# Kernel optimization log

Measured on AMD Instinct MI355X. Metric: run time of the kernel, lower is better.

Reference implementation:

```python
import jax, jax.numpy as jnp
import numpy as np

N = 100000      # nodes
E = 1600000     # edges
G = 1000        # graphs in the batch
D_IN, D_H, D_OUT = 128, 128, 64


def setup_inputs() -> dict:
    key = jax.random.key(0)
    ks = jax.random.split(key, 8)
    x = jax.random.normal(ks[0], (N, D_IN), jnp.float32)
    edge_index = jax.random.randint(ks[1], (2, E), 0, N, dtype=jnp.int32)
    batch = jnp.sort(jax.random.randint(ks[2], (N,), 0, G, dtype=jnp.int32))
    s_in = 1.0 / np.sqrt(D_IN)
    s_h = 1.0 / np.sqrt(D_H)
    return {
        "x": x,
        "edge_index": edge_index,
        "batch": batch,
        "W_emb": jax.random.normal(ks[3], (D_IN, D_H), jnp.float32) * s_in,
        "b_emb": jnp.zeros((D_H,), jnp.float32),
        "W1": jax.random.normal(ks[4], (D_H, D_H), jnp.float32) * s_h,
        "b1": jnp.zeros((D_H,), jnp.float32),
        "W2": jax.random.normal(ks[5], (D_H, D_H), jnp.float32) * s_h,
        "b2": jnp.zeros((D_H,), jnp.float32),
        "W3": jax.random.normal(ks[6], (D_H, D_OUT), jnp.float32) * s_h,
        "b3": jnp.zeros((D_OUT,), jnp.float32),
    }


def reference(x, edge_index, batch, W_emb, b_emb, W1, b1, W2, b2, W3, b3):
    # Eval mode: dropout is identity.
    n = x.shape[0]
    src, dst = edge_index[0], edge_index[1]
    # GCN symmetric normalization with self-loops (Kipf & Welling).
    deg = jax.ops.segment_sum(jnp.ones(src.shape[0], x.dtype), dst, num_segments=n) + 1.0
    dis = jax.lax.rsqrt(deg)                 # deg^{-1/2}, [N]
    edge_norm = dis[src] * dis[dst]          # [E]
    self_norm = dis * dis                    # self-loop weight = 1/deg, [N]

    def gcn_conv(h, W, b):
        h = h @ W                                         # [N, d_out]
        agg = jax.ops.segment_sum(h[src] * edge_norm[:, None], dst, num_segments=n)
        return agg + h * self_norm[:, None] + b

    h = x @ W_emb + b_emb
    h = jax.nn.relu(gcn_conv(h, W1, b1))
    h = jax.nn.relu(gcn_conv(h, W2, b2))
    h = gcn_conv(h, W3, b3)
    # global_add_pool over graph ids
    return jax.ops.segment_sum(h, batch, num_segments=G)
```

## Files before the change

kernel.cpp:

```cpp
#include <hip/hip_runtime.h>
#include <hip/hip_bf16.h>

#define NN 100000
#define NE 1600000
#define NG 1000
#define SMAX 48

typedef unsigned short u16;
typedef unsigned int u32;
typedef u16 u16x8 __attribute__((ext_vector_type(8)));
typedef u32 u32x4 __attribute__((ext_vector_type(4)));
typedef float f32x4 __attribute__((ext_vector_type(4)));
typedef __attribute__((ext_vector_type(8))) short s16x8;
typedef __attribute__((ext_vector_type(4))) float facc4;

__device__ __forceinline__ float bf2f(u16 u) {
    union { u32 i; float f; } c; c.i = ((u32)u) << 16; return c.f;
}
__device__ __forceinline__ u16 f2bf(float f) {
    __hip_bfloat16 h = __float2bfloat16(f);
    union { __hip_bfloat16 h; u16 u; } c; c.h = h; return c.u;
}
__device__ __forceinline__ int ntload(const int* p) { return __builtin_nontemporal_load(p); }

__global__ __launch_bounds__(256) void detect_kernel(const u32* __restrict__ xr, int* __restrict__ flag) {
    __shared__ int cnt[256];
    int c = 0;
    for (int i = threadIdx.x; i < 4096; i += 256) {
        u32 e = (xr[i] >> 7) & 0xFFu;
        if (e >= 110u && e <= 135u) c++;
    }
    cnt[threadIdx.x] = c;
    __syncthreads();
    for (int o = 128; o > 0; o >>= 1) {
        if (threadIdx.x < o) cnt[threadIdx.x] += cnt[threadIdx.x + o];
        __syncthreads();
    }
    if (threadIdx.x == 0) flag[0] = (cnt[0] > 2048) ? 1 : 0;
}

#define MEGA_NB 12726
__global__ __launch_bounds__(256) void mega_prep(
    const void* __restrict__ x, const int* __restrict__ flag, u16* __restrict__ xb,
    const void* __restrict__ Wemb, const void* __restrict__ W1, const void* __restrict__ W2,
    const void* __restrict__ W3, u16* __restrict__ wembT, u16* __restrict__ w1T,
    u16* __restrict__ w2T, u16* __restrict__ w3T,
    const void* __restrict__ bemb, const void* __restrict__ b1, const void* __restrict__ b2,
    const void* __restrict__ b3, float* __restrict__ bembF, float* __restrict__ b1F,
    float* __restrict__ b2F, float* __restrict__ b3F,
    const int* __restrict__ ei, int* __restrict__ counts)
{
    int b = blockIdx.x, tid = threadIdx.x;
    int fl = flag[0];
    if (b < 6250) {
        if (fl) return;
        int c = b * 256 + tid;
        f32x4 a = reinterpret_cast<const f32x4*>(x)[c * 2];
        f32x4 d = reinterpret_cast<const f32x4*>(x)[c * 2 + 1];
        u16x8 o;
        #pragma unroll
        for (int j = 0; j < 4; ++j) { o[j] = f2bf(a[j]); o[4 + j] = f2bf(d[j]); }
        reinterpret_cast<u16x8*>(xb)[c] = o;
    } else if (b < 6474) {
        int o = (b - 6250) * 256 + tid;
        const void* src; u16* dst; int M; int ol;
        if (o < 16384)      { src = Wemb; dst = wembT; M = 128; ol = o; }
        else if (o < 32768) { src = W1;   dst = w1T;   M = 128; ol = o - 16384; }
        else if (o < 49152) { src = W2;   dst = w2T;   M = 128; ol = o - 32768; }
        else                { src = W3;   dst = w3T;   M = 64;  ol = o - 49152; }
        int n = ol >> 7, k = ol & 127;
        u16 v = fl ? reinterpret_cast<const u16*>(src)[k * M + n]
                   : f2bf(reinterpret_cast<const float*>(src)[k * M + n]);
        dst[ol] = v;
    } else if (b < 6476) {
        int i = (b - 6474) * 256 + tid;
        if (i >= 448) return;
        const void* src; float* dst; int il;
        if (i < 128)      { src = bemb; dst = bembF; il = i; }
        else if (i < 256) { src = b1;   dst = b1F;   il = i - 128; }
        else if (i < 384) { src = b2;   dst = b2F;   il = i - 256; }
        else              { src = b3;   dst = b3F;   il = i - 384; }
        dst[il] = fl ? bf2f(reinterpret_cast<const u16*>(src)[il])
                     : reinterpret_cast<const float*>(src)[il];
    } else {
        int e = (b - 6476) * 256 + tid;
        if (e < NE) atomicAdd(&counts[ei[NE + e]], 1);
    }
}

__global__ __launch_bounds__(256) void wfuse_kernel(const u16* __restrict__ w1T, const u16* __restrict__ wembT,
                                                    const float* __restrict__ bembF,
                                                    u16* __restrict__ WfT, float* __restrict__ bfW) {
    int b = blockIdx.x;
    if (b < 64) {
        int o = b * 256 + threadIdx.x;
        int n = o >> 7, k = o & 127;
        float acc = 0.f;
        #pragma unroll 4
        for (int j = 0; j < 128; ++j)
            acc += bf2f(w1T[n * 128 + j]) * bf2f(wembT[j * 128 + k]);
        WfT[o] = f2bf(acc);
    } else {
        int n = threadIdx.x;
        if (n < 128) {
            float acc = 0.f;
            for (int j = 0; j < 128; ++j)
                acc += bembF[j] * bf2f(w1T[n * 128 + j]);
            bfW[n] = acc;
        }
    }
}

__global__ __launch_bounds__(256) void scan1_kernel(const int* __restrict__ counts, int* __restrict__ offs,
                                                    int* __restrict__ bsums, float* __restrict__ dis,
                                                    int* __restrict__ cursor) {
    __shared__ int sums[256];
    int tid = threadIdx.x;
    int base = blockIdx.x * 2048 + tid * 8;
    int local[8];
    int s = 0;
    #pragma unroll
    for (int i = 0; i < 8; ++i) {
        int v = 0;
        if (base + i < NN) {
            v = counts[base + i];
            dis[base + i] = rsqrtf((float)v + 1.0f);
            cursor[base + i] = 0;
        }
        local[i] = s; s += v;
    }
    sums[tid] = s;
    __syncthreads();
    for (int o = 1; o < 256; o <<= 1) {
        int v = (tid >= o) ? sums[tid - o] : 0;
        __syncthreads();
        sums[tid] += v;
        __syncthreads();
    }
    int excl = sums[tid] - s;
    #pragma unroll
    for (int i = 0; i < 8; ++i)
        if (base + i < NN) offs[base + i] = excl + local[i];
    if (tid == 255) bsums[blockIdx.x] = sums[255];
}

__global__ __launch_bounds__(256) void scan3_kernel(int* __restrict__ offs, const int* __restrict__ bsums) {
    __shared__ int addv;
    int i = blockIdx.x * 256 + threadIdx.x;
    int bucket = blockIdx.x >> 3;
    if (threadIdx.x == 0) {
        int s = 0;
        for (int k = 0; k < bucket; ++k) s += bsums[k];
        addv = s;
    }
    __syncthreads();
    if (i < NN) offs[i] += addv;
}

#define MEGA2_SCAT 6250
__global__ __launch_bounds__(256, 5) void mega2_kernel(
    const u16* __restrict__ xb, const u16* __restrict__ xraw, const int* __restrict__ flag,
    const u16* __restrict__ WfT, const float* __restrict__ bfW, u16* __restrict__ Hout,
    const int* __restrict__ ei, const int* __restrict__ offs, int* __restrict__ cursor,
    int* __restrict__ srcs)
{
    int b = blockIdx.x, tid = threadIdx.x;
    if (b < MEGA2_SCAT) {
        int e = b * 256 + tid;
        if (e < NE) {
            int s = ei[e], d = ei[NE + e];
            int pos = offs[d] + atomicAdd(&cursor[d], 1);
            srcs[pos] = s;
        }
    } else {
        const u16* A = flag[0] ? xraw : xb;
        int gb = b - MEGA2_SCAT;
        int wv = tid >> 6, lane = tid & 63;
        int m = lane & 15, quad = lane >> 4;
        int r0 = gb * 64 + wv * 16;
        int ar = r0 + m; if (ar >= NN) ar = NN - 1;
        facc4 acc[8];
        #pragma unroll
        for (int t = 0; t < 8; ++t) acc[t] = (facc4){0.f, 0.f, 0.f, 0.f};
        const u16* arow = A + (size_t)ar * 128 + quad * 8;
        #pragma unroll
        for (int k0 = 0; k0 < 128; k0 += 32) {
            s16x8 a = *reinterpret_cast<const s16x8*>(arow + k0);
            #pragma unroll
            for (int t = 0; t < 8; ++t) {
                s16x8 bfr = *reinterpret_cast<const s16x8*>(WfT + (t * 16 + m) * 128 + k0 + quad * 8);
                acc[t] = __builtin_amdgcn_mfma_f32_16x16x32_bf16(a, bfr, acc[t], 0, 0, 0);
            }
        }
        #pragma unroll
        for (int t = 0; t < 8; ++t) {
            int col = t * 16 + m;
            float bv = bfW[col];
            #pragma unroll
            for (int r = 0; r < 4; ++r) {
                int orow = r0 + quad * 4 + r;
                if (orow < NN)
                    Hout[(size_t)orow * 128 + col] = f2bf(acc[t][r] + bv);
            }
        }
    }
}

template <int MOUT>
__global__ __launch_bounds__(256) void fused_agg_gemm(const u16* __restrict__ T, const int* __restrict__ offs,
                                                      const int* __restrict__ counts, const float* __restrict__ dis,
                                                      const int* __restrict__ srcs, const float* __restrict__ aggbias,
                                                      const u16* __restrict__ Wt, u16* __restrict__ Hout) {
    constexpr int LDW = 136;
    __shared__ u16 sW[MOUT * LDW];
    __shared__ u16 sA[64 * LDW];
    int tid = threadIdx.x;
    for (int c = tid; c < MOUT * 16; c += 256) {
        int n = c >> 4, kc = (c & 15) << 3;
        *reinterpret_cast<u16x8*>(sW + n * LDW + kc) = reinterpret_cast<const u16x8*>(Wt)[c];
    }

    int lane = tid & 15, grp = tid >> 4;
    const u32x4* T4 = reinterpret_cast<const u32x4*>(T);
    for (int i = 0; i < 4; ++i) {
        int nl = grp * 4 + i;
        int n = blockIdx.x * 64 + nl;
        bool valid = n < NN;
        int nc = valid ? n : NN - 1;
        float di = dis[nc];
        float sn = di * di;
        u32x4 ts = T4[(size_t)nc * 16 + lane];
        float acc[8];
        #pragma unroll
        for (int q = 0; q < 4; ++q) {
            acc[2 * q]     = bf2f((u16)(ts[q] & 0xffffu)) * sn + aggbias[lane * 8 + 2 * q];
            acc[2 * q + 1] = bf2f((u16)(ts[q] >> 16))     * sn + aggbias[lane * 8 + 2 * q + 1];
        }
        int st = offs[nc], cnt = valid ? counts[nc] : 0;
        int j = 0;
        for (; j + 4 <= cnt; j += 4) {
            int e0 = ntload(srcs + st + j);
            int e1 = ntload(srcs + st + j + 1);
            int e2 = ntload(srcs + st + j + 2);
            int e3 = ntload(srcs + st + j + 3);
            float w0 = dis[e0] * di, w1 = dis[e1] * di, w2 = dis[e2] * di, w3 = dis[e3] * di;
            u32x4 g0 = T4[(size_t)e0 * 16 + lane];
            u32x4 g1 = T4[(size_t)e1 * 16 + lane];
            u32x4 g2 = T4[(size_t)e2 * 16 + lane];
            u32x4 g3 = T4[(size_t)e3 * 16 + lane];
            #pragma unroll
            for (int q = 0; q < 4; ++q) {
                acc[2 * q]     += bf2f((u16)(g0[q] & 0xffffu)) * w0;
                acc[2 * q + 1] += bf2f((u16)(g0[q] >> 16))     * w0;
                acc[2 * q]     += bf2f((u16)(g1[q] & 0xffffu)) * w1;
                acc[2 * q + 1] += bf2f((u16)(g1[q] >> 16))     * w1;
                acc[2 * q]     += bf2f((u16)(g2[q] & 0xffffu)) * w2;
                acc[2 * q + 1] += bf2f((u16)(g2[q] >> 16))     * w2;
                acc[2 * q]     += bf2f((u16)(g3[q] & 0xffffu)) * w3;
                acc[2 * q + 1] += bf2f((u16)(g3[q] >> 16))     * w3;
            }
        }
        for (; j < cnt; ++j) {
            int e = ntload(srcs + st + j);
            float w = dis[e] * di;
            u32x4 g = T4[(size_t)e * 16 + lane];
            #pragma unroll
            for (int q = 0; q < 4; ++q) {
                acc[2 * q]     += bf2f((u16)(g[q] & 0xffffu)) * w;
                acc[2 * q + 1] += bf2f((u16)(g[q] >> 16))     * w;
            }
        }
        u16x8 pk;
        #pragma unroll
        for (int q = 0; q < 4; ++q) {
            pk[2 * q]     = f2bf(fmaxf(acc[2 * q], 0.0f));
            pk[2 * q + 1] = f2bf(fmaxf(acc[2 * q + 1], 0.0f));
        }
        *reinterpret_cast<u16x8*>(sA + nl * LDW + lane * 8) = pk;
    }
    __syncthreads();

    int wv = tid >> 6, l64 = tid & 63;
    int m = l64 & 15, quad = l64 >> 4;
    int r0 = blockIdx.x * 64 + wv * 16;
    constexpr int NT = MOUT / 16;
    facc4 gacc[NT];
    #pragma unroll
    for (int t = 0; t < NT; ++t) gacc[t] = (facc4){0.f, 0.f, 0.f, 0.f};
    #pragma unroll
    for (int k0 = 0; k0 < 128; k0 += 32) {
        s16x8 a = *reinterpret_cast<const s16x8*>(sA + (wv * 16 + m) * LDW + k0 + quad * 8);
        #pragma unroll
        for (int t = 0; t < NT; ++t) {
            s16x8 bfr = *reinterpret_cast<const s16x8*>(sW + (t * 16 + m) * LDW + k0 + quad * 8);
            gacc[t] = __builtin_amdgcn_mfma_f32_16x16x32_bf16(a, bfr, gacc[t], 0, 0, 0);
        }
    }
    #pragma unroll
    for (int t = 0; t < NT; ++t) {
        int col = t * 16 + m;
        #pragma unroll
        for (int r = 0; r < 4; ++r) {
            int orow = r0 + quad * 4 + r;
            if (orow < NN)
                Hout[(size_t)orow * MOUT + col] = f2bf(gacc[t][r]);
        }
    }
}

__global__ __launch_bounds__(256) void agg_pool_kernel(const u16* __restrict__ T, const int* __restrict__ offs,
                                                       const int* __restrict__ counts, const float* __restrict__ dis,
                                                       const int* __restrict__ srcs, const float* __restrict__ bias,
                                                       const int* __restrict__ batch, float* __restrict__ outF) {
    __shared__ float accG[SMAX * 64];
    __shared__ int sg0;
    int tid = threadIdx.x;
    for (int i = tid; i < SMAX * 64; i += 256) accG[i] = 0.0f;
    if (tid == 0) sg0 = batch[blockIdx.x * 32];
    __syncthreads();
    int g0 = sg0;
    int lane = tid & 7;
    int n = blockIdx.x * 32 + (tid >> 3);

    const u32x4* T4 = reinterpret_cast<const u32x4*>(T);
    float di = dis[n];
    float sn = di * di;
    u32x4 ts = T4[(size_t)n * 8 + lane];
    float acc[8];
    #pragma unroll
    for (int q = 0; q < 4; ++q) {
        acc[2 * q]     = bf2f((u16)(ts[q] & 0xffffu)) * sn + bias[lane * 8 + 2 * q];
        acc[2 * q + 1] = bf2f((u16)(ts[q] >> 16))     * sn + bias[lane * 8 + 2 * q + 1];
    }
    int st = offs[n], cnt = counts[n];
    int j = 0;
    for (; j + 4 <= cnt; j += 4) {
        int e0 = ntload(srcs + st + j);
        int e1 = ntload(srcs + st + j + 1);
        int e2 = ntload(srcs + st + j + 2);
        int e3 = ntload(srcs + st + j + 3);
        float w0 = dis[e0] * di, w1 = dis[e1] * di, w2 = dis[e2] * di, w3 = dis[e3] * di;
        u32x4 g0v = T4[(size_t)e0 * 8 + lane];
        u32x4 g1v = T4[(size_t)e1 * 8 + lane];
        u32x4 g2v = T4[(size_t)e2 * 8 + lane];
        u32x4 g3v = T4[(size_t)e3 * 8 + lane];
        #pragma unroll
        for (int q = 0; q < 4; ++q) {
            acc[2 * q]     += bf2f((u16)(g0v[q] & 0xffffu)) * w0;
            acc[2 * q + 1] += bf2f((u16)(g0v[q] >> 16))     * w0;
            acc[2 * q]     += bf2f((u16)(g1v[q] & 0xffffu)) * w1;
            acc[2 * q + 1] += bf2f((u16)(g1v[q] >> 16))     * w1;
            acc[2 * q]     += bf2f((u16)(g2v[q] & 0xffffu)) * w2;
            acc[2 * q + 1] += bf2f((u16)(g2v[q] >> 16))     * w2;
            acc[2 * q]     += bf2f((u16)(g3v[q] & 0xffffu)) * w3;
            acc[2 * q + 1] += bf2f((u16)(g3v[q] >> 16))     * w3;
        }
    }
    for (; j < cnt; ++j) {
        int e = ntload(srcs + st + j);
        float w = dis[e] * di;
        u32x4 g = T4[(size_t)e * 8 + lane];
        #pragma unroll
        for (int q = 0; q < 4; ++q) {
            acc[2 * q]     += bf2f((u16)(g[q] & 0xffffu)) * w;
            acc[2 * q + 1] += bf2f((u16)(g[q] >> 16))     * w;
        }
    }

    int s = batch[n] - g0;
    if (s >= 0 && s < SMAX) {
        #pragma unroll
        for (int q = 0; q < 8; ++q)
            atomicAdd(&accG[s * 64 + lane * 8 + q], acc[q]);
    } else {
        #pragma unroll
        for (int q = 0; q < 8; ++q)
            atomicAdd(&outF[(size_t)(g0 + s) * 64 + lane * 8 + q], acc[q]);
    }
    __syncthreads();
    int gend = batch[blockIdx.x * 32 + 31];
    int span = gend - g0 + 1;
    if (span > SMAX) span = SMAX;
    for (int i = tid; i < span * 64; i += 256)
        atomicAdd(&outF[(size_t)g0 * 64 + i], accG[i]);
}

__global__ __launch_bounds__(256) void out_cvt_kernel(const float* __restrict__ outF, void* __restrict__ out,
                                                      const int* __restrict__ flag) {
    int i = blockIdx.x * 256 + threadIdx.x;
    if (i < NG * 64) {
        float v = outF[i];
        if (flag[0]) reinterpret_cast<u16*>(out)[i] = f2bf(v);
        else         reinterpret_cast<float*>(out)[i] = v;
    }
}

extern "C" void kernel_launch(void* const* d_in, const int* in_sizes, int n_in,
                              void* d_out, int out_size, void* d_ws, size_t ws_size,
                              hipStream_t stream) {
    const void* x     = d_in[0];
    const int* ei     = (const int*)d_in[1];
    const int* batch  = (const int*)d_in[2];
    const void* W_emb = d_in[3];
    const void* b_emb = d_in[4];
    const void* W1    = d_in[5];
    const void* b1    = d_in[6];
    const void* W2    = d_in[7];
    const void* b2    = d_in[8];
    const void* W3    = d_in[9];
    const void* b3    = d_in[10];

    char* p = (char*)d_ws;
    auto alloc = [&](size_t bytes) { void* r = p; p += (bytes + 255) & ~(size_t)255; return r; };
    int*   flag   = (int*)alloc(256);
    int*   counts = (int*)alloc(NN * 4);
    int*   cursor = (int*)alloc(NN * 4);
    int*   offs   = (int*)alloc(NN * 4);
    float* dis    = (float*)alloc(NN * 4);
    int*   bsums  = (int*)alloc(256 * 4);
    int*   srcs   = (int*)alloc((size_t)NE * 4);
    u16*   wembT  = (u16*)alloc(128 * 128 * 2);
    u16*   w1T    = (u16*)alloc(128 * 128 * 2);
    u16*   w2T    = (u16*)alloc(128 * 128 * 2);
    u16*   w3T    = (u16*)alloc(64 * 128 * 2);
    u16*   WfT    = (u16*)alloc(128 * 128 * 2);
    float* bembF  = (float*)alloc(128 * 4);
    float* b1F    = (float*)alloc(128 * 4);
    float* b2F    = (float*)alloc(128 * 4);
    float* b3F    = (float*)alloc(64 * 4);
    float* bfW    = (float*)alloc(128 * 4);
    float* outF   = (float*)alloc((size_t)NG * 64 * 4);
    u16*   hA     = (u16*)alloc((size_t)(NN + 64) * 128 * 2);
    u16*   hB     = (u16*)alloc((size_t)(NN + 64) * 128 * 2);

    hipMemsetAsync(counts, 0, NN * 4, stream);
    hipMemsetAsync(outF, 0, (size_t)NG * 64 * 4, stream);

    const int SB = (NN + 2047) / 2048;
    const int NB = (NN + 255) / 256;
    const int GB = (NN + 63) / 64;

    detect_kernel<<<1, 256, 0, stream>>>((const u32*)x, flag);
    mega_prep<<<MEGA_NB, 256, 0, stream>>>(x, flag, hB, W_emb, W1, W2, W3, wembT, w1T, w2T, w3T,
                                           b_emb, b1, b2, b3, bembF, b1F, b2F, b3F, ei, counts);
    wfuse_kernel<<<65, 256, 0, stream>>>(w1T, wembT, bembF, WfT, bfW);
    scan1_kernel<<<SB, 256, 0, stream>>>(counts, offs, bsums, dis, cursor);
    scan3_kernel<<<NB, 256, 0, stream>>>(offs, bsums);

    mega2_kernel<<<MEGA2_SCAT + GB, 256, 0, stream>>>(hB, (const u16*)x, flag, WfT, bfW, hA,
                                                      ei, offs, cursor, srcs);
    fused_agg_gemm<128><<<GB, 256, 0, stream>>>(hA, offs, counts, dis, srcs, b1F, w2T, hB);
    fused_agg_gemm<64><<<GB, 256, 0, stream>>>(hB, offs, counts, dis, srcs, b2F, w3T, hA);
    agg_pool_kernel<<<NN / 32, 256, 0, stream>>>(hA, offs, counts, dis, srcs, b3F, batch, outF);
    out_cvt_kernel<<<(NG * 64 + 255) / 256, 256, 0, stream>>>(outF, d_out, flag);
}
```

Baseline: 582.0 us.

## Precompute per-edge normalization into packed CSR and split scatter from embedding GEMM

The CSR scatter now stores (src, dis[src]*dis[dst]) pairs as int2, so the three aggregation kernels no longer do a dependent random gather of dis[src] per edge. The combined scatter/GEMM mega kernel is split into a separate scatter kernel and an embedding GEMM that stages the weights in shared memory. This doubles the edge-list footprint (8 bytes per edge instead of 4) and removes the overlap between scatter and GEMM that the combined launch allowed. The nontemporal load hints on the edge list are also dropped.

```diff
diff --git a/kernel.cpp b/kernel.cpp
--- a/kernel.cpp
+++ b/kernel.cpp
@@ -21,7 +21,6 @@
     __hip_bfloat16 h = __float2bfloat16(f);
     union { __hip_bfloat16 h; u16 u; } c; c.h = h; return c.u;
 }
-__device__ __forceinline__ int ntload(const int* p) { return __builtin_nontemporal_load(p); }
 
 __global__ __launch_bounds__(256) void detect_kernel(const u32* __restrict__ xr, int* __restrict__ flag) {
     __shared__ int cnt[256];
@@ -157,51 +156,57 @@
     if (i < NN) offs[i] += addv;
 }
 
-#define MEGA2_SCAT 6250
-__global__ __launch_bounds__(256, 5) void mega2_kernel(
-    const u16* __restrict__ xb, const u16* __restrict__ xraw, const int* __restrict__ flag,
-    const u16* __restrict__ WfT, const float* __restrict__ bfW, u16* __restrict__ Hout,
-    const int* __restrict__ ei, const int* __restrict__ offs, int* __restrict__ cursor,
-    int* __restrict__ srcs)
-{
-    int b = blockIdx.x, tid = threadIdx.x;
-    if (b < MEGA2_SCAT) {
-        int e = b * 256 + tid;
-        if (e < NE) {
-            int s = ei[e], d = ei[NE + e];
-            int pos = offs[d] + atomicAdd(&cursor[d], 1);
-            srcs[pos] = s;
-        }
-    } else {
-        const u16* A = flag[0] ? xraw : xb;
-        int gb = b - MEGA2_SCAT;
-        int wv = tid >> 6, lane = tid & 63;
-        int m = lane & 15, quad = lane >> 4;
-        int r0 = gb * 64 + wv * 16;
-        int ar = r0 + m; if (ar >= NN) ar = NN - 1;
-        facc4 acc[8];
-        #pragma unroll
-        for (int t = 0; t < 8; ++t) acc[t] = (facc4){0.f, 0.f, 0.f, 0.f};
-        const u16* arow = A + (size_t)ar * 128 + quad * 8;
-        #pragma unroll
-        for (int k0 = 0; k0 < 128; k0 += 32) {
-            s16x8 a = *reinterpret_cast<const s16x8*>(arow + k0);
-            #pragma unroll
-            for (int t = 0; t < 8; ++t) {
-                s16x8 bfr = *reinterpret_cast<const s16x8*>(WfT + (t * 16 + m) * 128 + k0 + quad * 8);
-                acc[t] = __builtin_amdgcn_mfma_f32_16x16x32_bf16(a, bfr, acc[t], 0, 0, 0);
-            }
-        }
+__global__ __launch_bounds__(256) void scatter_kernel(const int* __restrict__ ei, const int* __restrict__ offs,
+                                                      int* __restrict__ cursor, const float* __restrict__ dis,
+                                                      int2* __restrict__ edges) {
+    int e = blockIdx.x * 256 + threadIdx.x;
+    if (e < NE) {
+        int s = ei[e], d = ei[NE + e];
+        int pos = offs[d] + atomicAdd(&cursor[d], 1);
+        int2 pk;
+        pk.x = s;
+        pk.y = __float_as_int(dis[s] * dis[d]);
+        edges[pos] = pk;
+    }
+}
+
+__global__ __launch_bounds__(256) void gemm_emb(const u16* __restrict__ xb, const u16* __restrict__ xraw,
+                                                const int* __restrict__ flag, const u16* __restrict__ WfT,
+                                                const float* __restrict__ bfW, u16* __restrict__ Hout) {
+    __shared__ u16 sW[128 * 136];
+    int tid = threadIdx.x;
+    const u16* A = flag[0] ? xraw : xb;
+    for (int c = tid; c < 128 * 16; c += 256) {
+        int n = c >> 4, kc = (c & 15) << 3;
+        *reinterpret_cast<u16x8*>(sW + n * 136 + kc) = reinterpret_cast<const u16x8*>(WfT)[c];
+    }
+    __syncthreads();
+    int wv = tid >> 6, lane = tid & 63;
+    int m = lane & 15, quad = lane >> 4;
+    int r0 = blockIdx.x * 64 + wv * 16;
+    int ar = r0 + m; if (ar >= NN) ar = NN - 1;
+    facc4 acc[8];
+    #pragma unroll
+    for (int t = 0; t < 8; ++t) acc[t] = (facc4){0.f, 0.f, 0.f, 0.f};
+    const u16* arow = A + (size_t)ar * 128 + quad * 8;
+    #pragma unroll
+    for (int k0 = 0; k0 < 128; k0 += 32) {
+        s16x8 a = *reinterpret_cast<const s16x8*>(arow + k0);
         #pragma unroll
         for (int t = 0; t < 8; ++t) {
-            int col = t * 16 + m;
-            float bv = bfW[col];
-            #pragma unroll
-            for (int r = 0; r < 4; ++r) {
-                int orow = r0 + quad * 4 + r;
-                if (orow < NN)
-                    Hout[(size_t)orow * 128 + col] = f2bf(acc[t][r] + bv);
-            }
+            s16x8 bfr = *reinterpret_cast<const s16x8*>(sW + (t * 16 + m) * 136 + k0 + quad * 8);
+            acc[t] = __builtin_amdgcn_mfma_f32_16x16x32_bf16(a, bfr, acc[t], 0, 0, 0);
+        }
+    }
+    #pragma unroll
+    for (int t = 0; t < 8; ++t) {
+        int col = t * 16 + m;
+        float bv = bfW[col];
+        #pragma unroll
+        for (int r = 0; r < 4; ++r) {
+            int orow = r0 + quad * 4 + r;
+            if (orow < NN)
+                Hout[(size_t)orow * 128 + col] = f2bf(acc[t][r] + bv);
         }
     }
 }
@@ -209,7 +214,7 @@
 template <int MOUT>
 __global__ __launch_bounds__(256) void fused_agg_gemm(const u16* __restrict__ T, const int* __restrict__ offs,
                                                       const int* __restrict__ counts, const float* __restrict__ dis,
-                                                      const int* __restrict__ srcs, const float* __restrict__ aggbias,
+                                                      const int2* __restrict__ edges, const float* __restrict__ aggbias,
                                                       const u16* __restrict__ Wt, u16* __restrict__ Hout) {
     constexpr int LDW = 136;
     __shared__ u16 sW[MOUT * LDW];
@@ -239,15 +244,16 @@
         int st = offs[nc], cnt = valid ? counts[nc] : 0;
         int j = 0;
         for (; j + 4 <= cnt; j += 4) {
-            int e0 = ntload(srcs + st + j);
-            int e1 = ntload(srcs + st + j + 1);
-            int e2 = ntload(srcs + st + j + 2);
-            int e3 = ntload(srcs + st + j + 3);
-            float w0 = dis[e0] * di, w1 = dis[e1] * di, w2 = dis[e2] * di, w3 = dis[e3] * di;
-            u32x4 g0 = T4[(size_t)e0 * 16 + lane];
-            u32x4 g1 = T4[(size_t)e1 * 16 + lane];
-            u32x4 g2 = T4[(size_t)e2 * 16 + lane];
-            u32x4 g3 = T4[(size_t)e3 * 16 + lane];
+            int2 e0 = edges[st + j];
+            int2 e1 = edges[st + j + 1];
+            int2 e2 = edges[st + j + 2];
+            int2 e3 = edges[st + j + 3];
+            u32x4 g0 = T4[(size_t)e0.x * 16 + lane];
+            u32x4 g1 = T4[(size_t)e1.x * 16 + lane];
+            u32x4 g2 = T4[(size_t)e2.x * 16 + lane];
+            u32x4 g3 = T4[(size_t)e3.x * 16 + lane];
+            float w0 = __int_as_float(e0.y), w1 = __int_as_float(e1.y);
+            float w2 = __int_as_float(e2.y), w3 = __int_as_float(e3.y);
             #pragma unroll
             for (int q = 0; q < 4; ++q) {
                 acc[2 * q]     += bf2f((u16)(g0[q] & 0xffffu)) * w0;
@@ -261,9 +267,9 @@
             }
         }
         for (; j < cnt; ++j) {
-            int e = ntload(srcs + st + j);
-            float w = dis[e] * di;
-            u32x4 g = T4[(size_t)e * 16 + lane];
+            int2 e = edges[st + j];
+            u32x4 g = T4[(size_t)e.x * 16 + lane];
+            float w = __int_as_float(e.y);
             #pragma unroll
             for (int q = 0; q < 4; ++q) {
                 acc[2 * q]     += bf2f((u16)(g[q] & 0xffffu)) * w;
@@ -310,7 +316,7 @@
 
 __global__ __launch_bounds__(256) void agg_pool_kernel(const u16* __restrict__ T, const int* __restrict__ offs,
                                                        const int* __restrict__ counts, const float* __restrict__ dis,
-                                                       const int* __restrict__ srcs, const float* __restrict__ bias,
+                                                       const int2* __restrict__ edges, const float* __restrict__ bias,
                                                        const int* __restrict__ batch, float* __restrict__ outF) {
     __shared__ float accG[SMAX * 64];
     __shared__ int sg0;
@@ -335,15 +341,16 @@
     int st = offs[n], cnt = counts[n];
     int j = 0;
     for (; j + 4 <= cnt; j += 4) {
-        int e0 = ntload(srcs + st + j);
-        int e1 = ntload(srcs + st + j + 1);
-        int e2 = ntload(srcs + st + j + 2);
-        int e3 = ntload(srcs + st + j + 3);
-        float w0 = dis[e0] * di, w1 = dis[e1] * di, w2 = dis[e2] * di, w3 = dis[e3] * di;
-        u32x4 g0v = T4[(size_t)e0 * 8 + lane];
-        u32x4 g1v = T4[(size_t)e1 * 8 + lane];
-        u32x4 g2v = T4[(size_t)e2 * 8 + lane];
-        u32x4 g3v = T4[(size_t)e3 * 8 + lane];
+        int2 e0 = edges[st + j];
+        int2 e1 = edges[st + j + 1];
+        int2 e2 = edges[st + j + 2];
+        int2 e3 = edges[st + j + 3];
+        u32x4 g0v = T4[(size_t)e0.x * 8 + lane];
+        u32x4 g1v = T4[(size_t)e1.x * 8 + lane];
+        u32x4 g2v = T4[(size_t)e2.x * 8 + lane];
+        u32x4 g3v = T4[(size_t)e3.x * 8 + lane];
+        float w0 = __int_as_float(e0.y), w1 = __int_as_float(e1.y);
+        float w2 = __int_as_float(e2.y), w3 = __int_as_float(e3.y);
         #pragma unroll
         for (int q = 0; q < 4; ++q) {
             acc[2 * q]     += bf2f((u16)(g0v[q] & 0xffffu)) * w0;
@@ -357,9 +364,9 @@
         }
     }
     for (; j < cnt; ++j) {
-        int e = ntload(srcs + st + j);
-        float w = dis[e] * di;
-        u32x4 g = T4[(size_t)e * 8 + lane];
+        int2 e = edges[st + j];
+        u32x4 g = T4[(size_t)e.x * 8 + lane];
+        float w = __int_as_float(e.y);
         #pragma unroll
         for (int q = 0; q < 4; ++q) {
             acc[2 * q]     += bf2f((u16)(g[q] & 0xffffu)) * w;
@@ -418,7 +425,7 @@
     int*   offs   = (int*)alloc(NN * 4);
     float* dis    = (float*)alloc(NN * 4);
     int*   bsums  = (int*)alloc(256 * 4);
-    int*   srcs   = (int*)alloc((size_t)NE * 4);
+    int2*  edges  = (int2*)alloc((size_t)NE * 8);
     u16*   wembT  = (u16*)alloc(128 * 128 * 2);
     u16*   w1T    = (u16*)alloc(128 * 128 * 2);
     u16*   w2T    = (u16*)alloc(128 * 128 * 2);
@@ -439,6 +446,7 @@
     const int SB = (NN + 2047) / 2048;
     const int NB = (NN + 255) / 256;
     const int GB = (NN + 63) / 64;
+    const int EB = (NE + 255) / 256;
 
     detect_kernel<<<1, 256, 0, stream>>>((const u32*)x, flag);
     mega_prep<<<MEGA_NB, 256, 0, stream>>>(x, flag, hB, W_emb, W1, W2, W3, wembT, w1T, w2T, w3T,
@@ -446,11 +454,10 @@
     wfuse_kernel<<<65, 256, 0, stream>>>(w1T, wembT, bembF, WfT, bfW);
     scan1_kernel<<<SB, 256, 0, stream>>>(counts, offs, bsums, dis, cursor);
     scan3_kernel<<<NB, 256, 0, stream>>>(offs, bsums);
-
-    mega2_kernel<<<MEGA2_SCAT + GB, 256, 0, stream>>>(hB, (const u16*)x, flag, WfT, bfW, hA,
-                                                      ei, offs, cursor, srcs);
-    fused_agg_gemm<128><<<GB, 256, 0, stream>>>(hA, offs, counts, dis, srcs, b1F, w2T, hB);
-    fused_agg_gemm<64><<<GB, 256, 0, stream>>>(hB, offs, counts, dis, srcs, b2F, w3T, hA);
-    agg_pool_kernel<<<NN / 32, 256, 0, stream>>>(hA, offs, counts, dis, srcs, b3F, batch, outF);
+    scatter_kernel<<<EB, 256, 0, stream>>>(ei, offs, cursor, dis, edges);
+    gemm_emb<<<GB, 256, 0, stream>>>(hB, (const u16*)x, flag, WfT, bfW, hA);
+    fused_agg_gemm<128><<<GB, 256, 0, stream>>>(hA, offs, counts, dis, edges, b1F, w2T, hB);
+    fused_agg_gemm<64><<<GB, 256, 0, stream>>>(hB, offs, counts, dis, edges, b2F, w3T, hA);
+    agg_pool_kernel<<<NN / 32, 256, 0, stream>>>(hA, offs, counts, dis, edges, b3F, batch, outF);
     out_cvt_kernel<<<(NG * 64 + 255) / 256, 256, 0, stream>>>(outF, d_out, flag);
 }
```

New measurement: 515.0 us. -11.5%, faster.
